# Kernel optimization log

Hardware: AMD Instinct MI355X
Metric: run time of the kernel (lower is better)

The kernel has to match this reference:

```python
import jax, jax.numpy as jnp
import numpy as np

N_HEADS = 8
D_K = 64
SCALE = D_K ** -0.5


def setup_inputs() -> dict:
    key = jax.random.key(0)
    ks = jax.random.split(key, 5)
    B, C, H, W = 4, 512, 32, 32
    x = jax.random.normal(ks[0], (B, C, H, W), dtype=jnp.float32)
    Wp = jax.random.normal(ks[1], (3 * N_HEADS * D_K, C), dtype=jnp.float32) * (C ** -0.5)
    bp = jax.random.normal(ks[2], (3 * N_HEADS * D_K,), dtype=jnp.float32) * 0.02
    Wo = jax.random.normal(ks[3], (C, N_HEADS * D_K), dtype=jnp.float32) * ((N_HEADS * D_K) ** -0.5)
    bo = jax.random.normal(ks[4], (C,), dtype=jnp.float32) * 0.02
    return {"x": x, "Wp": Wp, "bp": bp, "Wo": Wo, "bo": bo}


def reference(x, Wp, bp, Wo, bo):
    # x: [B, C, H, W]; NOTE: the torch module defines GroupNorm but never calls it.
    B, C, H, W = x.shape
    s = H * W
    xs = x.reshape(B, C, s).transpose(0, 2, 1)          # [B, s, C]
    qkv = (xs @ Wp.T + bp).reshape(B, s, N_HEADS, 3 * D_K)
    q, k, v = jnp.split(qkv, 3, axis=-1)                 # each [B, s, h, d]
    attn = jnp.einsum('bihd,bjhd->bijh', q, k) * SCALE   # [B, s, s, h]
    attn = jax.nn.softmax(attn, axis=2)                  # softmax over j (keys)
    res = jnp.einsum('bijh,bjhd->bihd', attn, v)         # [B, s, h, d]
    res = res.reshape(B, s, N_HEADS * D_K)
    out = res @ Wo.T + bo + xs                           # residual add
    return out.transpose(0, 2, 1).reshape(B, C, H, W)
```

## Files before the change

### kernel.cpp

```cpp
#include <hip/hip_runtime.h>
#include <hip/hip_bf16.h>

typedef unsigned short u16;
typedef __attribute__((ext_vector_type(8))) short frag_ab;
typedef __attribute__((ext_vector_type(4))) float f32x4;
typedef _Float16 f16;
typedef __attribute__((ext_vector_type(4))) _Float16 f16x4;

#define LOG2E 1.44269504088896f

__device__ __forceinline__ float fast_exp2(float x) {
    return __builtin_amdgcn_exp2f(x);
}

__device__ __forceinline__ void gload_lds16(const u16* g, u16* s) {
    __builtin_amdgcn_global_load_lds((const __attribute__((address_space(1))) void*)g,
                                     (__attribute__((address_space(3))) void*)s, 16, 0, 0);
}
__device__ __forceinline__ void gload_lds16h(const f16* g, f16* s) {
    __builtin_amdgcn_global_load_lds((const __attribute__((address_space(1))) void*)g,
                                     (__attribute__((address_space(3))) void*)s, 16, 0, 0);
}

__device__ __forceinline__ void gemm64x128_bt_mainloop(
    const u16* __restrict__ A, const u16* __restrict__ B, int K,
    int m0, int n0, f32x4 acc[2][4], u16* As, u16* Bs)
{
    const int tid = threadIdx.x;
    const int lane = tid & 63, quad = lane >> 4, l16 = lane & 15;
    const int wr = ((tid >> 7) & 1) * 32;
    const int wc = ((tid >> 6) & 1) * 64;
    const int srow = tid >> 3;
    const int scol = (tid & 7) * 8;

    for (int k0 = 0; k0 < K; k0 += 64) {
        __syncthreads();
        #pragma unroll
        for (int p = 0; p < 2; ++p) {
            const int r = srow + p * 32;
            gload_lds16(A + (size_t)(m0 + r) * K + k0 + scol, As + r * 64 + scol);
        }
        #pragma unroll
        for (int p = 0; p < 4; ++p) {
            const int r = srow + p * 32;
            gload_lds16(B + (size_t)(n0 + r) * K + k0 + scol, Bs + r * 64 + scol);
        }
        __syncthreads();
        #pragma unroll
        for (int ks = 0; ks < 2; ++ks) {
            frag_ab a[2], b[4];
            #pragma unroll
            for (int mt = 0; mt < 2; ++mt)
                a[mt] = *(const frag_ab*)(As + (wr + mt * 16 + l16) * 64 + ks * 32 + quad * 8);
            #pragma unroll
            for (int nt = 0; nt < 4; ++nt)
                b[nt] = *(const frag_ab*)(Bs + (wc + nt * 16 + l16) * 64 + ks * 32 + quad * 8);
            #pragma unroll
            for (int mt = 0; mt < 2; ++mt)
                #pragma unroll
                for (int nt = 0; nt < 4; ++nt)
                    acc[mt][nt] = __builtin_amdgcn_mfma_f32_16x16x32_bf16(a[mt], b[nt], acc[mt][nt], 0, 0, 0);
        }
    }
}

__device__ __forceinline__ void gemm64x64_bt_mainloop(
    const u16* __restrict__ A, const u16* __restrict__ B, int K,
    int m0, int n0, f32x4 acc[2][2], u16* As, u16* Bs)
{
    const int tid = threadIdx.x;
    const int lane = tid & 63, quad = lane >> 4, l16 = lane & 15;
    const int wr = ((tid >> 7) & 1) * 32;
    const int wc = ((tid >> 6) & 1) * 32;
    const int srow = tid >> 3;
    const int scol = (tid & 7) * 8;

    for (int k0 = 0; k0 < K; k0 += 64) {
        __syncthreads();
        #pragma unroll
        for (int p = 0; p < 2; ++p) {
            const int r = srow + p * 32;
            gload_lds16(A + (size_t)(m0 + r) * K + k0 + scol, As + r * 64 + scol);
            gload_lds16(B + (size_t)(n0 + r) * K + k0 + scol, Bs + r * 64 + scol);
        }
        __syncthreads();
        #pragma unroll
        for (int ks = 0; ks < 2; ++ks) {
            frag_ab a[2], b[2];
            #pragma unroll
            for (int mt = 0; mt < 2; ++mt)
                a[mt] = *(const frag_ab*)(As + (wr + mt * 16 + l16) * 64 + ks * 32 + quad * 8);
            #pragma unroll
            for (int nt = 0; nt < 2; ++nt)
                b[nt] = *(const frag_ab*)(Bs + (wc + nt * 16 + l16) * 64 + ks * 32 + quad * 8);
            #pragma unroll
            for (int mt = 0; mt < 2; ++mt)
                #pragma unroll
                for (int nt = 0; nt < 2; ++nt)
                    acc[mt][nt] = __builtin_amdgcn_mfma_f32_16x16x32_bf16(a[mt], b[nt], acc[mt][nt], 0, 0, 0);
        }
    }
}

__global__ __launch_bounds__(256) void prep_kernel(
    const float* __restrict__ x, __hip_bfloat16* __restrict__ xs_bf,
    const float* __restrict__ Wp, const float* __restrict__ Wo,
    __hip_bfloat16* __restrict__ w_bf)
{
    __shared__ float tile[32][33];
    const int tid = threadIdx.x;
    const int id = blockIdx.x;
    if (id < 2048) {
        const int i0 = (id & 31) * 32;
        const int c0 = ((id >> 5) & 15) * 32;
        const int b  = id >> 9;
        const int tx = tid & 31, ty = tid >> 5;
        const float* xp = x + ((size_t)b * 512 + c0) * 1024 + i0;
        #pragma unroll
        for (int r = ty; r < 32; r += 8)
            tile[r][tx] = xp[(size_t)r * 1024 + tx];
        __syncthreads();
        __hip_bfloat16* op = xs_bf + ((size_t)b * 1024 + i0) * 512 + c0;
        #pragma unroll
        for (int r = ty; r < 32; r += 8)
            op[(size_t)r * 512 + tx] = __float2bfloat16(tile[tx][r]);
    } else {
        const int t = (id - 2048) * 256 + tid;
        const int i4 = t * 4;
        const float* src = (i4 < 786432) ? (Wp + i4) : (Wo + (i4 - 786432));
        const float4 v = *(const float4*)src;
        ushort4 o;
        o.x = __bfloat16_as_ushort(__float2bfloat16(v.x));
        o.y = __bfloat16_as_ushort(__float2bfloat16(v.y));
        o.z = __bfloat16_as_ushort(__float2bfloat16(v.z));
        o.w = __bfloat16_as_ushort(__float2bfloat16(v.w));
        *(ushort4*)((u16*)w_bf + i4) = o;
    }
}

__global__ __launch_bounds__(256) void qkv_gemm_kernel(
    const u16* __restrict__ Wpb, const u16* __restrict__ xsb,
    const float* __restrict__ bp,
    u16* __restrict__ Qb, u16* __restrict__ Kb, f16* __restrict__ VtT)
{
    __shared__ u16 lds[12288];
    u16* As = lds;
    u16* Bs = lds + 4096;
    f32x4 acc[2][4];
    #pragma unroll
    for (int mt = 0; mt < 2; ++mt)
        #pragma unroll
        for (int nt = 0; nt < 4; ++nt)
            { acc[mt][nt][0]=0.f; acc[mt][nt][1]=0.f; acc[mt][nt][2]=0.f; acc[mt][nt][3]=0.f; }
    const int m0 = blockIdx.y * 64;
    const int n0 = blockIdx.x * 128;
    gemm64x128_bt_mainloop(Wpb, xsb, 512, m0, n0, acc, As, Bs);

    const int tid = threadIdx.x;
    const int lane = tid & 63, quad = lane >> 4, l16 = lane & 15;
    const int wr = ((tid >> 7) & 1) * 32, wc = ((tid >> 6) & 1) * 64;
    const int h = blockIdx.y / 3, part = blockIdx.y % 3;
    const int b = blockIdx.x >> 3, ipb = (blockIdx.x & 7) * 128;
    const size_t bh = (size_t)(b * 8 + h);

    if (part < 2) {
        const float scale = (part == 0) ? (0.125f * LOG2E) : 1.0f;
        __syncthreads();
        u16* T = lds;
        #pragma unroll
        for (int nt = 0; nt < 4; ++nt) {
            const int px = wc + nt * 16 + l16;
            #pragma unroll
            for (int mt = 0; mt < 2; ++mt) {
                const int cb = m0 + wr + mt * 16 + quad * 4;
                ushort4 pk;
                pk.x = __bfloat16_as_ushort(__float2bfloat16((acc[mt][nt][0] + bp[cb + 0]) * scale));
                pk.y = __bfloat16_as_ushort(__float2bfloat16((acc[mt][nt][1] + bp[cb + 1]) * scale));
                pk.z = __bfloat16_as_ushort(__float2bfloat16((acc[mt][nt][2] + bp[cb + 2]) * scale));
                pk.w = __bfloat16_as_ushort(__float2bfloat16((acc[mt][nt][3] + bp[cb + 3]) * scale));
                *(ushort4*)&T[px * 72 + wr + mt * 16 + quad * 4] = pk;
            }
        }
        __syncthreads();
        u16* dst = (part == 0 ? Qb : Kb);
        #pragma unroll
        for (int p = 0; p < 4; ++p) {
            const int row = p * 32 + (tid >> 3);
            const int ch8 = (tid & 7) * 8;
            uint4 rv = *(uint4*)&T[row * 72 + ch8];
            *(uint4*)(dst + ((bh * 1024 + ipb + row) << 6) + ch8) = rv;
        }
    } else {
        f16* dst = VtT + bh * 65536;
        #pragma unroll
        for (int mt = 0; mt < 2; ++mt) {
            #pragma unroll
            for (int r = 0; r < 4; ++r) {
                const int d = wr + mt * 16 + quad * 4 + r;
                const float bias = bp[m0 + d];
                #pragma unroll
                for (int nt = 0; nt < 4; ++nt) {
                    const int j = ipb + wc + nt * 16 + l16;
                    dst[(size_t)(j >> 3) * 512 + d * 8 + (j & 7)] =
                        (f16)(acc[mt][nt][r] + bias);
                }
            }
        }
    }
}

__global__ __launch_bounds__(256) void attn_kernel(
    const u16* __restrict__ Qb, const u16* __restrict__ Kb,
    const f16* __restrict__ VtT, __hip_bfloat16* __restrict__ resb)
{
    __shared__ u16 Ks[128 * 64];
    __shared__ f16 Vs[16 * 64 * 8];
    __shared__ float Opart[4][32][68];
    __shared__ float Lpart[4][4][16];
    const int bh = blockIdx.x;
    const int it = blockIdx.y;
    const int tid = threadIdx.x;
    const int w = tid >> 6, lane = tid & 63, quad = lane >> 4, l16 = lane & 15;
    const int srow = tid >> 3, scol = (tid & 7) * 8;

    const u16* Qp = Qb + (size_t)bh * 65536;
    const u16* Kp = Kb + (size_t)bh * 65536;
    const f16* Vp = VtT + (size_t)bh * 65536;

    frag_ab bq[4][2];
    #pragma unroll
    for (int ig = 0; ig < 4; ++ig) {
        const u16* qptr = Qp + (size_t)(it * 64 + ig * 16 + l16) * 64 + quad * 8;
        bq[ig][0] = *(const frag_ab*)(qptr);
        bq[ig][1] = *(const frag_ab*)(qptr + 32);
    }

    f32x4 o[4][4];
    #pragma unroll
    for (int ig = 0; ig < 4; ++ig)
        #pragma unroll
        for (int dt = 0; dt < 4; ++dt)
            { o[ig][dt][0]=0.f; o[ig][dt][1]=0.f; o[ig][dt][2]=0.f; o[ig][dt][3]=0.f; }
    float l_acc[4] = {0.f, 0.f, 0.f, 0.f};

    for (int jt = 0; jt < 8; ++jt) {
        __syncthreads();
        #pragma unroll
        for (int p = 0; p < 4; ++p) {
            const int r = srow + p * 32;
            gload_lds16(Kp + (size_t)(jt * 128 + r) * 64 + scol, Ks + r * 64 + scol);
        }
        #pragma unroll
        for (int p = 0; p < 4; ++p) {
            const int c = w * 4 + p;
            gload_lds16h(Vp + (size_t)((jt * 16 + c) * 64 + lane) * 8,
                         Vs + (size_t)(c * 64 + lane) * 8);
        }
        __syncthreads();

        frag_ab ka[2][2];
        #pragma unroll
        for (int mt = 0; mt < 2; ++mt) {
            const u16* kp = Ks + (w * 32 + mt * 16 + l16) * 64 + quad * 8;
            ka[mt][0] = *(const frag_ab*)(kp);
            ka[mt][1] = *(const frag_ab*)(kp + 32);
        }
        f16x4 va[4][2];
        #pragma unroll
        for (int ks = 0; ks < 2; ++ks) {
            const f16* vrow = Vs + (size_t)(w * 4 + ks * 2 + (quad >> 1)) * 512 + (quad & 1) * 4;
            #pragma unroll
            for (int dt = 0; dt < 4; ++dt)
                va[dt][ks] = *(const f16x4*)(vrow + (dt * 16 + l16) * 8);
        }
        #pragma unroll
        for (int ig = 0; ig < 4; ++ig) {
            f32x4 st0 = {0.f, 0.f, 0.f, 0.f}, st1 = {0.f, 0.f, 0.f, 0.f};
            st0 = __builtin_amdgcn_mfma_f32_16x16x32_bf16(ka[0][0], bq[ig][0], st0, 0, 0, 0);
            st0 = __builtin_amdgcn_mfma_f32_16x16x32_bf16(ka[0][1], bq[ig][1], st0, 0, 0, 0);
            st1 = __builtin_amdgcn_mfma_f32_16x16x32_bf16(ka[1][0], bq[ig][0], st1, 0, 0, 0);
            st1 = __builtin_amdgcn_mfma_f32_16x16x32_bf16(ka[1][1], bq[ig][1], st1, 0, 0, 0);
            f16x4 p0, p1;
            float s = 0.f;
            #pragma unroll
            for (int r = 0; r < 4; ++r) {
                const float e0 = fast_exp2(st0[r]);
                const float e1 = fast_exp2(st1[r]);
                s += e0 + e1;
                p0[r] = (f16)e0;
                p1[r] = (f16)e1;
            }
            l_acc[ig] += s;
            #pragma unroll
            for (int dt = 0; dt < 4; ++dt) {
                o[ig][dt] = __builtin_amdgcn_mfma_f32_16x16x16f16(va[dt][0], p0, o[ig][dt], 0, 0, 0);
                o[ig][dt] = __builtin_amdgcn_mfma_f32_16x16x16f16(va[dt][1], p1, o[ig][dt], 0, 0, 0);
            }
        }
    }
    #pragma unroll
    for (int ig = 0; ig < 4; ++ig) {
        l_acc[ig] += __shfl_xor(l_acc[ig], 16);
        l_acc[ig] += __shfl_xor(l_acc[ig], 32);
    }
    if (lane < 16) {
        #pragma unroll
        for (int ig = 0; ig < 4; ++ig)
            Lpart[w][ig][lane] = l_acc[ig];
    }

    const int bb = bh >> 3, hh = bh & 7;
    const int il = tid >> 3, d0 = (tid & 7) * 8;
    #pragma unroll
    for (int ph = 0; ph < 2; ++ph) {
        __syncthreads();
        #pragma unroll
        for (int g = 0; g < 2; ++g) {
            const int ig = ph * 2 + g;
            #pragma unroll
            for (int dt = 0; dt < 4; ++dt)
                *(f32x4*)&Opart[w][g * 16 + l16][dt * 16 + quad * 4] = o[ig][dt];
        }
        __syncthreads();
        f32x4 sa = *(const f32x4*)&Opart[0][il][d0];
        f32x4 sb = *(const f32x4*)&Opart[0][il][d0 + 4];
        #pragma unroll
        for (int ww = 1; ww < 4; ++ww) {
            sa += *(const f32x4*)&Opart[ww][il][d0];
            sb += *(const f32x4*)&Opart[ww][il][d0 + 4];
        }
        const int ig = ph * 2 + (il >> 4);
        const float linv = 1.f / (Lpart[0][ig][il & 15] + Lpart[1][ig][il & 15] +
                                  Lpart[2][ig][il & 15] + Lpart[3][ig][il & 15]);
        u16 pk[8];
        #pragma unroll
        for (int e = 0; e < 4; ++e) {
            pk[e]     = __bfloat16_as_ushort(__float2bfloat16(sa[e] * linv));
            pk[e + 4] = __bfloat16_as_ushort(__float2bfloat16(sb[e] * linv));
        }
        u16* orow = (u16*)resb +
            ((size_t)(bb * 1024 + it * 64 + ph * 32 + il)) * 512 + hh * 64 + d0;
        *(uint4*)orow = *(uint4*)pk;
    }
}

__global__ __launch_bounds__(256) void out_gemm_kernel(
    const u16* __restrict__ Wob, const u16* __restrict__ resb,
    const float* __restrict__ bo, const float* __restrict__ x,
    float* __restrict__ out)
{
    __shared__ u16 As[64 * 64];
    __shared__ u16 Bs[64 * 64];
    f32x4 acc[2][2];
    #pragma unroll
    for (int mt = 0; mt < 2; ++mt)
        #pragma unroll
        for (int nt = 0; nt < 2; ++nt)
            { acc[mt][nt][0]=0.f; acc[mt][nt][1]=0.f; acc[mt][nt][2]=0.f; acc[mt][nt][3]=0.f; }
    const int m0 = blockIdx.x * 64;
    const int n0 = blockIdx.y * 64;
    gemm64x64_bt_mainloop(Wob, resb, 512, m0, n0, acc, As, Bs);

    const int tid = threadIdx.x;
    const int lane = tid & 63, quad = lane >> 4, l16 = lane & 15;
    const int wr = ((tid >> 7) & 1) * 32, wc = ((tid >> 6) & 1) * 32;
    #pragma unroll
    for (int nt = 0; nt < 2; ++nt) {
        const int pix = n0 + wc + nt * 16 + l16;
        const int b = pix >> 10, ip = pix & 1023;
        #pragma unroll
        for (int mt = 0; mt < 2; ++mt) {
            #pragma unroll
            for (int r = 0; r < 4; ++r) {
                const int c = m0 + wr + mt * 16 + quad * 4 + r;
                const size_t oidx = (((size_t)b * 512 + c) << 10) + ip;
                out[oidx] = acc[mt][nt][r] + bo[c] + x[oidx];
            }
        }
    }
}

extern "C" void kernel_launch(void* const* d_in, const int* in_sizes, int n_in,
                              void* d_out, int out_size, void* d_ws, size_t ws_size,
                              hipStream_t stream)
{
    const float* x  = (const float*)d_in[0];
    const float* Wp = (const float*)d_in[1];
    const float* bp = (const float*)d_in[2];
    const float* Wo = (const float*)d_in[3];
    const float* bo = (const float*)d_in[4];
    float* out = (float*)d_out;

    char* ws = (char*)d_ws;
    size_t off = 0;
    auto carve = [&](size_t bytes) -> void* {
        void* ptr = ws + off;
        off += (bytes + 255) & ~(size_t)255;
        return ptr;
    };
    __hip_bfloat16* xs_bf = (__hip_bfloat16*)carve((size_t)4096 * 512 * 2);
    __hip_bfloat16* Wp_bf = (__hip_bfloat16*)carve((size_t)1536 * 512 * 2);
    __hip_bfloat16* Wo_bf = (__hip_bfloat16*)carve((size_t)512 * 512 * 2);
    u16*            Qb    = (u16*)carve((size_t)32 * 1024 * 64 * 2);
    u16*            Kb    = (u16*)carve((size_t)32 * 1024 * 64 * 2);
    f16*            VtT   = (f16*)carve((size_t)32 * 1024 * 64 * 2);
    __hip_bfloat16* resb  = (__hip_bfloat16*)carve((size_t)4096 * 512 * 2);

    prep_kernel<<<dim3(3072), 256, 0, stream>>>(x, xs_bf, Wp, Wo, Wp_bf);
    qkv_gemm_kernel<<<dim3(32, 24), 256, 0, stream>>>(
        (const u16*)Wp_bf, (const u16*)xs_bf, bp, Qb, Kb, VtT);
    attn_kernel<<<dim3(32, 16), 256, 0, stream>>>(Qb, Kb, VtT, resb);
    out_gemm_kernel<<<dim3(8, 64), 256, 0, stream>>>(
        (const u16*)Wo_bf, (const u16*)resb, bo, x, out);
    (void)Wo_bf; (void)ws_size; (void)in_sizes; (void)n_in; (void)out_size;
}
```

Baseline: 115.2 us.

## Load K/V fragments directly from global into registers with double buffering

Replaces the LDS-staged K/V tiles and the two block-wide barriers per key tile with direct per-wave global loads into register fragments. Double-buffered register sets let the next tile's loads overlap the current tile's MFMAs. It also adds a launch-bounds occupancy hint of 2 blocks per CU. In exchange it raises register pressure and relies on L2/L1 for K/V reuse across the four query groups, with scattered 8-byte V loads.

```diff
diff --git a/kernel.cpp b/kernel.cpp
--- a/kernel.cpp
+++ b/kernel.cpp
@@ -14,10 +14,6 @@
 }
 
 __device__ __forceinline__ void gload_lds16(const u16* g, u16* s) {
-    __builtin_amdgcn_global_load_lds((const __attribute__((address_space(1))) void*)g,
-                                     (__attribute__((address_space(3))) void*)s, 16, 0, 0);
-}
-__device__ __forceinline__ void gload_lds16h(const f16* g, f16* s) {
     __builtin_amdgcn_global_load_lds((const __attribute__((address_space(1))) void*)g,
                                      (__attribute__((address_space(3))) void*)s, 16, 0, 0);
 }
@@ -209,19 +205,16 @@
     }
 }
 
-__global__ __launch_bounds__(256) void attn_kernel(
+__global__ __launch_bounds__(256, 2) void attn_kernel(
     const u16* __restrict__ Qb, const u16* __restrict__ Kb,
     const f16* __restrict__ VtT, __hip_bfloat16* __restrict__ resb)
 {
-    __shared__ u16 Ks[128 * 64];
-    __shared__ f16 Vs[16 * 64 * 8];
     __shared__ float Opart[4][32][68];
     __shared__ float Lpart[4][4][16];
     const int bh = blockIdx.x;
     const int it = blockIdx.y;
     const int tid = threadIdx.x;
     const int w = tid >> 6, lane = tid & 63, quad = lane >> 4, l16 = lane & 15;
-    const int srow = tid >> 3, scol = (tid & 7) * 8;
 
     const u16* Qp = Qb + (size_t)bh * 65536;
     const u16* Kp = Kb + (size_t)bh * 65536;
@@ -243,61 +236,64 @@
             { o[ig][dt][0]=0.f; o[ig][dt][1]=0.f; o[ig][dt][2]=0.f; o[ig][dt][3]=0.f; }
     float l_acc[4] = {0.f, 0.f, 0.f, 0.f};
 
-    for (int jt = 0; jt < 8; ++jt) {
-        __syncthreads();
-        #pragma unroll
-        for (int p = 0; p < 4; ++p) {
-            const int r = srow + p * 32;
-            gload_lds16(Kp + (size_t)(jt * 128 + r) * 64 + scol, Ks + r * 64 + scol);
-        }
-        #pragma unroll
-        for (int p = 0; p < 4; ++p) {
-            const int c = w * 4 + p;
-            gload_lds16h(Vp + (size_t)((jt * 16 + c) * 64 + lane) * 8,
-                         Vs + (size_t)(c * 64 + lane) * 8);
-        }
-        __syncthreads();
-
-        frag_ab ka[2][2];
-        #pragma unroll
-        for (int mt = 0; mt < 2; ++mt) {
-            const u16* kp = Ks + (w * 32 + mt * 16 + l16) * 64 + quad * 8;
-            ka[mt][0] = *(const frag_ab*)(kp);
-            ka[mt][1] = *(const frag_ab*)(kp + 32);
-        }
-        f16x4 va[4][2];
-        #pragma unroll
-        for (int ks = 0; ks < 2; ++ks) {
-            const f16* vrow = Vs + (size_t)(w * 4 + ks * 2 + (quad >> 1)) * 512 + (quad & 1) * 4;
-            #pragma unroll
-            for (int dt = 0; dt < 4; ++dt)
-                va[dt][ks] = *(const f16x4*)(vrow + (dt * 16 + l16) * 8);
-        }
-        #pragma unroll
-        for (int ig = 0; ig < 4; ++ig) {
-            f32x4 st0 = {0.f, 0.f, 0.f, 0.f}, st1 = {0.f, 0.f, 0.f, 0.f};
-            st0 = __builtin_amdgcn_mfma_f32_16x16x32_bf16(ka[0][0], bq[ig][0], st0, 0, 0, 0);
-            st0 = __builtin_amdgcn_mfma_f32_16x16x32_bf16(ka[0][1], bq[ig][1], st0, 0, 0, 0);
-            st1 = __builtin_amdgcn_mfma_f32_16x16x32_bf16(ka[1][0], bq[ig][0], st1, 0, 0, 0);
-            st1 = __builtin_amdgcn_mfma_f32_16x16x32_bf16(ka[1][1], bq[ig][1], st1, 0, 0, 0);
-            f16x4 p0, p1;
-            float s = 0.f;
-            #pragma unroll
-            for (int r = 0; r < 4; ++r) {
-                const float e0 = fast_exp2(st0[r]);
-                const float e1 = fast_exp2(st1[r]);
-                s += e0 + e1;
-                p0[r] = (f16)e0;
-                p1[r] = (f16)e1;
-            }
-            l_acc[ig] += s;
-            #pragma unroll
-            for (int dt = 0; dt < 4; ++dt) {
-                o[ig][dt] = __builtin_amdgcn_mfma_f32_16x16x16f16(va[dt][0], p0, o[ig][dt], 0, 0, 0);
-                o[ig][dt] = __builtin_amdgcn_mfma_f32_16x16x16f16(va[dt][1], p1, o[ig][dt], 0, 0, 0);
-            }
-        }
-    }
+    const u16* kbase = Kp + (size_t)(w * 32 + l16) * 64 + quad * 8;
+    const f16* vbase = Vp + (size_t)(w * 4 + (quad >> 1)) * 512 + l16 * 8 + (quad & 1) * 4;
+
+#define LOADKV(JT, KA, VA) do {                                              \
+        const u16* kp_ = kbase + (size_t)(JT) * 8192;                        \
+        KA[0][0] = *(const frag_ab*)(kp_);                                   \
+        KA[0][1] = *(const frag_ab*)(kp_ + 32);                              \
+        KA[1][0] = *(const frag_ab*)(kp_ + 1024);                            \
+        KA[1][1] = *(const frag_ab*)(kp_ + 1056);                            \
+        const f16* vp_ = vbase + (size_t)(JT) * 8192;                        \
+        _Pragma("unroll")                                                    \
+        for (int dt_ = 0; dt_ < 4; ++dt_) {                                  \
+            VA[dt_][0] = *(const f16x4*)(vp_ + dt_ * 128);                   \
+            VA[dt_][1] = *(const f16x4*)(vp_ + 1024 + dt_ * 128);            \
+        }                                                                    \
+    } while (0)
+
+#define COMPUTE(KA, VA) do {                                                 \
+        _Pragma("unroll")                                                    \
+        for (int ig = 0; ig < 4; ++ig) {                                     \
+            f32x4 st0 = {0.f, 0.f, 0.f, 0.f}, st1 = {0.f, 0.f, 0.f, 0.f};    \
+            st0 = __builtin_amdgcn_mfma_f32_16x16x32_bf16(KA[0][0], bq[ig][0], st0, 0, 0, 0); \
+            st0 = __builtin_amdgcn_mfma_f32_16x16x32_bf16(KA[0][1], bq[ig][1], st0, 0, 0, 0); \
+            st1 = __builtin_amdgcn_mfma_f32_16x16x32_bf16(KA[1][0], bq[ig][0], st1, 0, 0, 0); \
+            st1 = __builtin_amdgcn_mfma_f32_16x16x32_bf16(KA[1][1], bq[ig][1], st1, 0, 0, 0); \
+            f16x4 p0, p1;                                                    \
+            float s = 0.f;                                                   \
+            _Pragma("unroll")                                                \
+            for (int r = 0; r < 4; ++r) {                                    \
+                const float e0 = fast_exp2(st0[r]);                          \
+                const float e1 = fast_exp2(st1[r]);                          \
+                s += e0 + e1;                                                \
+                p0[r] = (f16)e0;                                             \
+                p1[r] = (f16)e1;                                             \
+            }                                                                \
+            l_acc[ig] += s;                                                  \
+            _Pragma("unroll")                                                \
+            for (int dt = 0; dt < 4; ++dt) {                                 \
+                o[ig][dt] = __builtin_amdgcn_mfma_f32_16x16x16f16(VA[dt][0], p0, o[ig][dt], 0, 0, 0); \
+                o[ig][dt] = __builtin_amdgcn_mfma_f32_16x16x16f16(VA[dt][1], p1, o[ig][dt], 0, 0, 0); \
+            }                                                                \
+        }                                                                    \
+    } while (0)
+
+    frag_ab ka0[2][2], ka1[2][2];
+    f16x4 va0[4][2], va1[4][2];
+    LOADKV(0, ka0, va0);
+    #pragma unroll
+    for (int jt = 0; jt < 8; jt += 2) {
+        LOADKV(jt + 1, ka1, va1);
+        COMPUTE(ka0, va0);
+        if (jt < 6)
+            LOADKV(jt + 2, ka0, va0);
+        COMPUTE(ka1, va1);
+    }
+#undef LOADKV
+#undef COMPUTE
+
     #pragma unroll
     for (int ig = 0; ig < 4; ++ig) {
         l_acc[ig] += __shfl_xor(l_acc[ig], 16);
```

New measurement: 114.5 us. No clear change (-0.6%).
